# Optimization experiments

Measured on AMD Instinct MI355X. Metric: run time of the kernel, lower is better.

Reference implementation:

```python
import math
import jax, jax.numpy as jnp
import numpy as np


def setup_inputs() -> dict:
    key = jax.random.key(0)
    ks = jax.random.split(key, 5)
    B, T, C = 4, 2048, 1024
    H = 16
    s = 0.02
    return {
        "x": jax.random.normal(ks[0], (B, T, C), dtype=jnp.float32),
        "W_attn": jax.random.normal(ks[1], (C, 3 * C), dtype=jnp.float32) * s,
        "b_attn": jax.random.normal(ks[2], (3 * C,), dtype=jnp.float32) * s,
        "W_proj": jax.random.normal(ks[3], (C, C), dtype=jnp.float32) * s,
        "b_proj": jax.random.normal(ks[4], (C,), dtype=jnp.float32) * s,
        "n_head": 16,
    }


def reference(x, W_attn, b_attn, W_proj, b_proj, n_head):
    B, T, C = x.shape
    hd = C // n_head
    qkv = x @ W_attn + b_attn  # (B,T,3C)
    q, k, v = jnp.split(qkv, 3, axis=-1)
    # (B,H,T,hd)
    q = q.reshape(B, T, n_head, hd).transpose(0, 2, 1, 3)
    k = k.reshape(B, T, n_head, hd).transpose(0, 2, 1, 3)
    v = v.reshape(B, T, n_head, hd).transpose(0, 2, 1, 3)
    # ||q-k||^2 = |q|^2 + |k|^2 - 2 q.k  (GEMM form, avoids (B,H,T,T,hd) diff tensor)
    q2 = jnp.sum(q * q, axis=-1)[..., :, None]  # (B,H,T,1)
    k2 = jnp.sum(k * k, axis=-1)[..., None, :]  # (B,H,1,T)
    qk = jnp.einsum("bhqd,bhkd->bhqk", q, k)    # (B,H,T,T)
    sq_l2 = q2 + k2 - 2.0 * qk
    scale = -1.0 / (2.0 * math.sqrt(hd))
    scores = jnp.exp(sq_l2 * scale)
    causal = jnp.tril(jnp.ones((T, T), dtype=bool))  # (T,T)
    scores = jnp.where(causal[None, None, :, :], scores, 0.0)
    y = jnp.einsum("bhqk,bhkd->bhqd", scores, v)  # (B,H,T,hd)
    y = y.transpose(0, 2, 1, 3).reshape(B, T, C)
    return y @ W_proj + b_proj
```

## Files before the change

kernel.cpp:

```cpp
#include <hip/hip_runtime.h>

typedef __bf16 bf16;
typedef __bf16 bf16x8 __attribute__((ext_vector_type(8)));
typedef float floatx4 __attribute__((ext_vector_type(4)));

#define MFMA_BF16(a, b, c) __builtin_amdgcn_mfma_f32_16x16x32_bf16((a), (b), (c), 0, 0, 0)

#define GLOAD_LDS16(gp, lp)                                      \
  __builtin_amdgcn_global_load_lds(                              \
      (const __attribute__((address_space(1))) void*)(gp),       \
      (__attribute__((address_space(3))) void*)(lp), 16, 0, 0)

#define SEQ_T 2048
#define DIM_C 1024
#define HDIM 64
#define MROWS 8192
#define N_QKV 3072

__global__ __launch_bounds__(256) void f32_to_bf16(
    const float* __restrict__ in, bf16* __restrict__ out) {
  const size_t i = ((size_t)blockIdx.x * 256 + threadIdx.x) * 8;
  const float4 f0 = *(const float4*)&in[i];
  const float4 f1 = *(const float4*)&in[i + 4];
  bf16x8 v;
  v[0] = (bf16)f0.x; v[1] = (bf16)f0.y; v[2] = (bf16)f0.z; v[3] = (bf16)f0.w;
  v[4] = (bf16)f1.x; v[5] = (bf16)f1.y; v[6] = (bf16)f1.z; v[7] = (bf16)f1.w;
  *(bf16x8*)&out[i] = v;
}

__global__ __launch_bounds__(256) void transpose_f32_bf16(
    const float* __restrict__ in, bf16* __restrict__ out, int R, int C) {
  __shared__ bf16 tile[32][33];
  const int bx = blockIdx.x * 32, by = blockIdx.y * 32;
  const int tx = threadIdx.x & 31, ty = threadIdx.x >> 5;
  for (int i = 0; i < 32; i += 8)
    tile[ty + i][tx] = (bf16)in[(size_t)(by + ty + i) * C + bx + tx];
  __syncthreads();
  for (int i = 0; i < 32; i += 8)
    out[(size_t)(bx + ty + i) * R + by + tx] = tile[tx][ty + i];
}

template <typename OT>
__global__ __launch_bounds__(256) void gemm_lds(
    const bf16* __restrict__ A,
    const bf16* __restrict__ Bt,
    const float* __restrict__ bias,
    OT* __restrict__ Cout,
    int M, int N, int K) {
  __shared__ __align__(16) bf16 Asl[128 * 64];
  __shared__ __align__(16) bf16 Bsl[128 * 64];
  const int bm = blockIdx.y * 128, bn = blockIdx.x * 128;
  const int tid = threadIdx.x;
  const int wave = tid >> 6, lane = tid & 63;
  const int wm = (wave >> 1) * 64, wn = (wave & 1) * 64;
  const int quad = lane >> 4, l16 = lane & 15;

  const floatx4 zero = {0.f, 0.f, 0.f, 0.f};
  floatx4 acc[4][4];
  for (int i = 0; i < 4; i++)
    for (int j = 0; j < 4; j++) acc[i][j] = zero;

  const bf16 *gA[4], *gB[4];
  bf16 *lA[4], *lB[4];
  for (int i = 0; i < 4; i++) {
    const int s = i * 256 + tid;
    const int row = s >> 3;
    const int c = (s & 7) ^ (row & 7);
    gA[i] = &A[(size_t)(bm + row) * K + c * 8];
    gB[i] = &Bt[(size_t)(bn + row) * K + c * 8];
    lA[i] = &Asl[(i * 256 + wave * 64) * 8];
    lB[i] = &Bsl[(i * 256 + wave * 64) * 8];
  }

  for (int k0 = 0; k0 < K; k0 += 64) {
    for (int i = 0; i < 4; i++) GLOAD_LDS16(gA[i] + k0, lA[i]);
    for (int i = 0; i < 4; i++) GLOAD_LDS16(gB[i] + k0, lB[i]);
    __syncthreads();
    for (int kk = 0; kk < 2; kk++) {
      bf16x8 af[4], bfr[4];
      for (int it = 0; it < 4; it++) {
        const int row = wm + it * 16 + l16;
        const int phys = (kk * 4 + quad) ^ (row & 7);
        af[it] = *(const bf16x8*)&Asl[row * 64 + phys * 8];
      }
      for (int jt = 0; jt < 4; jt++) {
        const int row = wn + jt * 16 + l16;
        const int phys = (kk * 4 + quad) ^ (row & 7);
        bfr[jt] = *(const bf16x8*)&Bsl[row * 64 + phys * 8];
      }
      for (int it = 0; it < 4; it++)
        for (int jt = 0; jt < 4; jt++)
          acc[it][jt] = MFMA_BF16(af[it], bfr[jt], acc[it][jt]);
    }
    __syncthreads();
  }
  for (int jt = 0; jt < 4; jt++) {
    const int col = bn + wn + jt * 16 + l16;
    const float bv = bias[col];
    for (int it = 0; it < 4; it++)
      for (int r = 0; r < 4; r++) {
        const int row = bm + wm + it * 16 + quad * 4 + r;
        Cout[(size_t)row * N + col] = (OT)(acc[it][jt][r] + bv);
      }
  }
}

__global__ __launch_bounds__(256, 4) void attn_kernel(
    const bf16* __restrict__ qkv,
    bf16* __restrict__ y) {
  const int p = blockIdx.x;
  const int bh = blockIdx.y;
  const int bb = bh >> 4, h = bh & 15;
  const int qtA = p, qtB = 31 - p;
  const int tid = threadIdx.x;
  const int wave = tid >> 6, lane = tid & 63;
  const int quad = lane >> 4, l16 = lane & 15;

  __shared__ __align__(16) bf16 Ps[128][72];
  __shared__ __align__(16) bf16 Ks[64][72];
  __shared__ __align__(16) bf16 Vt[64][72];
  __shared__ float q2c[128];

  const size_t rowbase = (size_t)bb * SEQ_T;
  const float c2 = -0.09016844f;
  const float m2c2 = 0.18033688f;

  bf16x8 aq[2][2];
  for (int T = 0; T < 2; T++) {
    const int qt = T ? qtB : qtA;
    const size_t grow = rowbase + qt * 64 + wave * 16 + l16;
    float s = 0.f;
    for (int ks = 0; ks < 2; ks++) {
      aq[T][ks] = *(const bf16x8*)&qkv[grow * N_QKV + h * HDIM + ks * 32 + quad * 8];
      for (int j = 0; j < 8; j++) { const float f = (float)aq[T][ks][j]; s += f * f; }
    }
    s += __shfl_xor(s, 16); s += __shfl_xor(s, 32);
    if (quad == 0) q2c[T * 64 + wave * 16 + l16] = s * c2;
  }

  const floatx4 zero = {0.f, 0.f, 0.f, 0.f};
  floatx4 accy[2][4];
  for (int T = 0; T < 2; T++)
    for (int jt = 0; jt < 4; jt++) accy[T][jt] = zero;

  for (int kt = 0; kt <= qtB; kt++) {
    const bool actA = (kt <= qtA);
    {
      const int r0 = tid >> 3, c8 = (tid & 7) << 3;
      for (int i = 0; i < 2; i++) {
        const int r = r0 + i * 32;
        const size_t gr = rowbase + (size_t)(kt * 64 + r);
        const bf16x8 kv = *(const bf16x8*)&qkv[gr * N_QKV + 1024 + h * HDIM + c8];
        *(bf16x8*)&Ks[r][c8] = kv;
        float s = 0.f;
        for (int j = 0; j < 8; j++) { const float f = (float)kv[j]; s += f * f; }
        s += __shfl_xor(s, 1); s += __shfl_xor(s, 2); s += __shfl_xor(s, 4);
        const float vscale = exp2f(s * c2);
        const bf16x8 vv = *(const bf16x8*)&qkv[gr * N_QKV + 2048 + h * HDIM + c8];
        for (int j = 0; j < 8; j++)
          Vt[c8 + j][r ^ c8] = (bf16)((float)vv[j] * vscale);
      }
    }
    __syncthreads();

    bf16x8 bk[4][2];
    for (int jt = 0; jt < 4; jt++)
      for (int ks = 0; ks < 2; ks++)
        bk[jt][ks] = *(const bf16x8*)&Ks[jt * 16 + l16][ks * 32 + quad * 8];
    floatx4 accs[2][4];
    for (int T = 0; T < 2; T++)
      for (int jt = 0; jt < 4; jt++) accs[T][jt] = zero;
    for (int T = 0; T < 2; T++) {
      if (T == 0 && !actA) continue;
      for (int ks = 0; ks < 2; ks++)
        for (int jt = 0; jt < 4; jt++)
          accs[T][jt] = MFMA_BF16(aq[T][ks], bk[jt][ks], accs[T][jt]);
    }

    for (int T = 0; T < 2; T++) {
      if (T == 0 && !actA) continue;
      const bool diag = (kt == (T == 0 ? qtA : qtB));
      for (int jt = 0; jt < 4; jt++) {
        const int nl = jt * 16 + l16;
        for (int r = 0; r < 4; r++) {
          const int ml = wave * 16 + quad * 4 + r;
          float pe = exp2f(m2c2 * accs[T][jt][r]);
          if (diag && nl > ml) pe = 0.f;
          Ps[T * 64 + ml][nl] = (bf16)pe;
        }
      }
    }

    bf16x8 bv[4][2];
    for (int jt = 0; jt < 4; jt++)
      for (int ks = 0; ks < 2; ks++) {
        const int d = jt * 16 + l16;
        bv[jt][ks] = *(const bf16x8*)&Vt[d][(ks * 32 + quad * 8) ^ (d & 0x38)];
      }
    for (int T = 0; T < 2; T++) {
      if (T == 0 && !actA) continue;
      for (int ks = 0; ks < 2; ks++) {
        const bf16x8 ap =
            *(const bf16x8*)&Ps[T * 64 + wave * 16 + l16][ks * 32 + quad * 8];
        for (int jt = 0; jt < 4; jt++)
          accy[T][jt] = MFMA_BF16(ap, bv[jt][ks], accy[T][jt]);
      }
    }
    __syncthreads();
  }

  for (int T = 0; T < 2; T++) {
    const int qt = (T == 0) ? qtA : qtB;
    float ysc[4];
    for (int r = 0; r < 4; r++)
      ysc[r] = exp2f(q2c[T * 64 + wave * 16 + quad * 4 + r]);
    for (int jt = 0; jt < 4; jt++) {
      const int col = h * HDIM + jt * 16 + l16;
      for (int r = 0; r < 4; r++) {
        const int ml = wave * 16 + quad * 4 + r;
        y[(rowbase + qt * 64 + ml) * DIM_C + col] = (bf16)(accy[T][jt][r] * ysc[r]);
      }
    }
  }
}

extern "C" void kernel_launch(void* const* d_in, const int* in_sizes, int n_in,
                              void* d_out, int out_size, void* d_ws, size_t ws_size,
                              hipStream_t stream) {
  const float* x      = (const float*)d_in[0];
  const float* W_attn = (const float*)d_in[1];
  const float* b_attn = (const float*)d_in[2];
  const float* W_proj = (const float*)d_in[3];
  const float* b_proj = (const float*)d_in[4];
  float* out = (float*)d_out;

  char* ws = (char*)d_ws;
  bf16* qkv = (bf16*)(ws);
  bf16* yb  = (bf16*)(ws + 50331648);
  bf16* WaT = (bf16*)(ws + 67108864);
  bf16* WpT = (bf16*)(ws + 73400320);
  bf16* xb  = yb;

  f32_to_bf16<<<dim3(4096), 256, 0, stream>>>(x, xb);
  transpose_f32_bf16<<<dim3(96, 32), 256, 0, stream>>>(W_attn, WaT, 1024, 3072);
  transpose_f32_bf16<<<dim3(32, 32), 256, 0, stream>>>(W_proj, WpT, 1024, 1024);
  gemm_lds<bf16><<<dim3(24, 64), 256, 0, stream>>>(
      xb, WaT, b_attn, qkv, MROWS, N_QKV, DIM_C);
  attn_kernel<<<dim3(16, 64), 256, 0, stream>>>(qkv, yb);
  gemm_lds<float><<<dim3(8, 64), 256, 0, stream>>>(
      yb, WpT, b_proj, out, MROWS, DIM_C, DIM_C);
}
```

Baseline: 302.8 us.

## Keep attention probabilities in registers, feed PV via 16x16x16 MFMA

```diff
diff --git a/kernel.cpp b/kernel.cpp
--- a/kernel.cpp
+++ b/kernel.cpp
@@ -2,9 +2,20 @@
 
 typedef __bf16 bf16;
 typedef __bf16 bf16x8 __attribute__((ext_vector_type(8)));
+typedef __bf16 bf16x4 __attribute__((ext_vector_type(4)));
+typedef short shortx4 __attribute__((ext_vector_type(4)));
 typedef float floatx4 __attribute__((ext_vector_type(4)));
 
 #define MFMA_BF16(a, b, c) __builtin_amdgcn_mfma_f32_16x16x32_bf16((a), (b), (c), 0, 0, 0)
+
+#if __has_builtin(__builtin_amdgcn_mfma_f32_16x16x16_bf16)
+#define MFMA16(a, b, c) __builtin_amdgcn_mfma_f32_16x16x16_bf16((a), (b), (c), 0, 0, 0)
+#else
+#define MFMA16(a, b, c)                                                   \
+  __builtin_amdgcn_mfma_f32_16x16x16bf16_1k(                              \
+      __builtin_bit_cast(shortx4, (a)), __builtin_bit_cast(shortx4, (b)), \
+      (c), 0, 0, 0)
+#endif
 
 #define GLOAD_LDS16(gp, lp)                                      \
   __builtin_amdgcn_global_load_lds(                              \
@@ -116,7 +127,6 @@
   const int wave = tid >> 6, lane = tid & 63;
   const int quad = lane >> 4, l16 = lane & 15;
 
-  __shared__ __align__(16) bf16 Ps[128][72];
   __shared__ __align__(16) bf16 Ks[64][72];
   __shared__ __align__(16) bf16 Vt[64][72];
   __shared__ float q2c[128];
@@ -141,7 +151,7 @@
   const floatx4 zero = {0.f, 0.f, 0.f, 0.f};
   floatx4 accy[2][4];
   for (int T = 0; T < 2; T++)
-    for (int jt = 0; jt < 4; jt++) accy[T][jt] = zero;
+    for (int dt = 0; dt < 4; dt++) accy[T][dt] = zero;
 
   for (int kt = 0; kt <= qtB; kt++) {
     const bool actA = (kt <= qtA);
@@ -164,47 +174,60 @@
     __syncthreads();
 
     bf16x8 bk[4][2];
+#pragma unroll
     for (int jt = 0; jt < 4; jt++)
+#pragma unroll
       for (int ks = 0; ks < 2; ks++)
         bk[jt][ks] = *(const bf16x8*)&Ks[jt * 16 + l16][ks * 32 + quad * 8];
     floatx4 accs[2][4];
+#pragma unroll
     for (int T = 0; T < 2; T++)
+#pragma unroll
       for (int jt = 0; jt < 4; jt++) accs[T][jt] = zero;
+#pragma unroll
     for (int T = 0; T < 2; T++) {
       if (T == 0 && !actA) continue;
+#pragma unroll
       for (int ks = 0; ks < 2; ks++)
+#pragma unroll
         for (int jt = 0; jt < 4; jt++)
-          accs[T][jt] = MFMA_BF16(aq[T][ks], bk[jt][ks], accs[T][jt]);
-    }
-
+          accs[T][jt] = MFMA_BF16(bk[jt][ks], aq[T][ks], accs[T][jt]);
+    }
+
+    bf16x4 ap[2][4];
+    const int qrow = wave * 16 + l16;
+#pragma unroll
     for (int T = 0; T < 2; T++) {
       if (T == 0 && !actA) continue;
       const bool diag = (kt == (T == 0 ? qtA : qtB));
+#pragma unroll
       for (int jt = 0; jt < 4; jt++) {
-        const int nl = jt * 16 + l16;
+        const int kb = jt * 16 + quad * 4;
+#pragma unroll
         for (int r = 0; r < 4; r++) {
-          const int ml = wave * 16 + quad * 4 + r;
           float pe = exp2f(m2c2 * accs[T][jt][r]);
-          if (diag && nl > ml) pe = 0.f;
-          Ps[T * 64 + ml][nl] = (bf16)pe;
+          if (diag && kb + r > qrow) pe = 0.f;
+          ap[T][jt][r] = (bf16)pe;
         }
       }
     }
 
-    bf16x8 bv[4][2];
-    for (int jt = 0; jt < 4; jt++)
-      for (int ks = 0; ks < 2; ks++) {
-        const int d = jt * 16 + l16;
-        bv[jt][ks] = *(const bf16x8*)&Vt[d][(ks * 32 + quad * 8) ^ (d & 0x38)];
-      }
-    for (int T = 0; T < 2; T++) {
-      if (T == 0 && !actA) continue;
-      for (int ks = 0; ks < 2; ks++) {
-        const bf16x8 ap =
-            *(const bf16x8*)&Ps[T * 64 + wave * 16 + l16][ks * 32 + quad * 8];
-        for (int jt = 0; jt < 4; jt++)
-          accy[T][jt] = MFMA_BF16(ap, bv[jt][ks], accy[T][jt]);
-      }
+#pragma unroll
+    for (int dt = 0; dt < 4; dt++) {
+      const int d = dt * 16 + l16;
+      const int swz = d & 0x38;
+      bf16x4 bv[4];
+#pragma unroll
+      for (int ksl = 0; ksl < 4; ksl++)
+        bv[ksl] = *(const bf16x4*)&Vt[d][(ksl * 16 + quad * 4) ^ swz];
+      if (actA) {
+#pragma unroll
+        for (int ksl = 0; ksl < 4; ksl++)
+          accy[0][dt] = MFMA16(ap[0][ksl], bv[ksl], accy[0][dt]);
+      }
+#pragma unroll
+      for (int ksl = 0; ksl < 4; ksl++)
+        accy[1][dt] = MFMA16(ap[1][ksl], bv[ksl], accy[1][dt]);
     }
     __syncthreads();
   }
@@ -214,11 +237,11 @@
     float ysc[4];
     for (int r = 0; r < 4; r++)
       ysc[r] = exp2f(q2c[T * 64 + wave * 16 + quad * 4 + r]);
-    for (int jt = 0; jt < 4; jt++) {
-      const int col = h * HDIM + jt * 16 + l16;
+    for (int dt = 0; dt < 4; dt++) {
+      const int col = h * HDIM + dt * 16 + l16;
       for (int r = 0; r < 4; r++) {
         const int ml = wave * 16 + quad * 4 + r;
-        y[(rowbase + qt * 64 + ml) * DIM_C + col] = (bf16)(accy[T][jt][r] * ysc[r]);
+        y[(rowbase + qt * 64 + ml) * DIM_C + col] = (bf16)(accy[T][dt][r] * ysc[r]);
       }
     }
   }
```

Result: slower. 353.2 us (+16.7%).

## Precompute scaled transposed V and double-buffer K/V loads in attention

Applied to the files above, without the earlier changes.

```diff
diff --git a/kernel.cpp b/kernel.cpp
--- a/kernel.cpp
+++ b/kernel.cpp
@@ -2,6 +2,7 @@
 
 typedef __bf16 bf16;
 typedef __bf16 bf16x8 __attribute__((ext_vector_type(8)));
+typedef __bf16 bf16x4 __attribute__((ext_vector_type(4)));
 typedef float floatx4 __attribute__((ext_vector_type(4)));
 
 #define MFMA_BF16(a, b, c) __builtin_amdgcn_mfma_f32_16x16x32_bf16((a), (b), (c), 0, 0, 0)
@@ -40,13 +41,43 @@
     out[(size_t)(bx + ty + i) * R + by + tx] = tile[tx][ty + i];
 }
 
+__global__ __launch_bounds__(256) void scale_transpose_v(
+    const bf16* __restrict__ qkv, bf16* __restrict__ VT) {
+  const int bh = blockIdx.x;
+  const int kt = blockIdx.y;
+  const int bb = bh >> 4, h = bh & 15;
+  const int tid = threadIdx.x;
+  __shared__ bf16 tile[64][72];
+  const int r0 = tid >> 3, c8 = (tid & 7) << 3;
+  const float c2 = -0.09016844f;
+  for (int i = 0; i < 2; i++) {
+    const int r = r0 + i * 32;
+    const size_t gr = (size_t)bb * SEQ_T + kt * 64 + r;
+    const bf16x8 kv = *(const bf16x8*)&qkv[gr * N_QKV + 1024 + h * HDIM + c8];
+    float s = 0.f;
+    for (int j = 0; j < 8; j++) { const float f = (float)kv[j]; s += f * f; }
+    s += __shfl_xor(s, 1); s += __shfl_xor(s, 2); s += __shfl_xor(s, 4);
+    const float vscale = exp2f(s * c2);
+    const bf16x8 vv = *(const bf16x8*)&qkv[gr * N_QKV + 2048 + h * HDIM + c8];
+    for (int j = 0; j < 8; j++)
+      tile[c8 + j][r ^ c8] = (bf16)((float)vv[j] * vscale);
+  }
+  __syncthreads();
+  for (int i = 0; i < 2; i++) {
+    const int u = i * 256 + tid;
+    const int d = u >> 3, kc = (u & 7) << 3;
+    const bf16x8 ov = *(const bf16x8*)&tile[d][kc ^ (d & 0x38)];
+    *(bf16x8*)&VT[(size_t)bh * 131072 + (size_t)d * 2048 + kt * 64 + kc] = ov;
+  }
+}
+
 template <typename OT>
 __global__ __launch_bounds__(256) void gemm_lds(
     const bf16* __restrict__ A,
     const bf16* __restrict__ Bt,
     const float* __restrict__ bias,
     OT* __restrict__ Cout,
-    int M, int N, int K) {
+    int M, int N, int K, int lda) {
   __shared__ __align__(16) bf16 Asl[128 * 64];
   __shared__ __align__(16) bf16 Bsl[128 * 64];
   const int bm = blockIdx.y * 128, bn = blockIdx.x * 128;
@@ -66,7 +97,7 @@
     const int s = i * 256 + tid;
     const int row = s >> 3;
     const int c = (s & 7) ^ (row & 7);
-    gA[i] = &A[(size_t)(bm + row) * K + c * 8];
+    gA[i] = &A[(size_t)(bm + row) * lda + c * 8];
     gB[i] = &Bt[(size_t)(bn + row) * K + c * 8];
     lA[i] = &Asl[(i * 256 + wave * 64) * 8];
     lB[i] = &Bsl[(i * 256 + wave * 64) * 8];
@@ -106,10 +137,10 @@
 }
 
 __global__ __launch_bounds__(256, 4) void attn_kernel(
-    const bf16* __restrict__ qkv,
-    bf16* __restrict__ y) {
-  const int p = blockIdx.x;
-  const int bh = blockIdx.y;
+    bf16* __restrict__ qkv,
+    const bf16* __restrict__ VT) {
+  const int p = blockIdx.y;
+  const int bh = blockIdx.x;
   const int bb = bh >> 4, h = bh & 15;
   const int qtA = p, qtB = 31 - p;
   const int tid = threadIdx.x;
@@ -117,8 +148,8 @@
   const int quad = lane >> 4, l16 = lane & 15;
 
   __shared__ __align__(16) bf16 Ps[128][72];
-  __shared__ __align__(16) bf16 Ks[64][72];
-  __shared__ __align__(16) bf16 Vt[64][72];
+  __shared__ __align__(16) bf16 Ksl[2][64 * 64];
+  __shared__ __align__(16) bf16 Vsl[2][64 * 64];
   __shared__ float q2c[128];
 
   const size_t rowbase = (size_t)bb * SEQ_T;
@@ -143,30 +174,38 @@
   for (int T = 0; T < 2; T++)
     for (int jt = 0; jt < 4; jt++) accy[T][jt] = zero;
 
+  const int r0 = tid >> 3;
+  const int cb = (tid & 7) ^ (r0 & 7);
+  const bf16* gK = &qkv[(rowbase + r0) * N_QKV + 1024 + h * HDIM + cb * 8];
+  const bf16* gV = &VT[(size_t)bh * 131072 + (size_t)r0 * 2048 + cb * 8];
+
+#define STAGE(kt_, nb_) do {                                            \
+    const size_t ko = (size_t)(kt_) * 64 * N_QKV;                       \
+    const int vo = (kt_) * 64;                                          \
+    GLOAD_LDS16(gK + ko,                    &Ksl[nb_][(wave * 64) * 8]);\
+    GLOAD_LDS16(gK + ko + (size_t)32 * N_QKV,                           \
+                &Ksl[nb_][(256 + wave * 64) * 8]);                      \
+    GLOAD_LDS16(gV + vo,                    &Vsl[nb_][(wave * 64) * 8]);\
+    GLOAD_LDS16(gV + vo + 32 * 2048,        &Vsl[nb_][(256 + wave * 64) * 8]);\
+  } while (0)
+
+  STAGE(0, 0);
+  int cur = 0;
+  const int qrow = wave * 16 + l16;
+
   for (int kt = 0; kt <= qtB; kt++) {
     const bool actA = (kt <= qtA);
-    {
-      const int r0 = tid >> 3, c8 = (tid & 7) << 3;
-      for (int i = 0; i < 2; i++) {
-        const int r = r0 + i * 32;
-        const size_t gr = rowbase + (size_t)(kt * 64 + r);
-        const bf16x8 kv = *(const bf16x8*)&qkv[gr * N_QKV + 1024 + h * HDIM + c8];
-        *(bf16x8*)&Ks[r][c8] = kv;
-        float s = 0.f;
-        for (int j = 0; j < 8; j++) { const float f = (float)kv[j]; s += f * f; }
-        s += __shfl_xor(s, 1); s += __shfl_xor(s, 2); s += __shfl_xor(s, 4);
-        const float vscale = exp2f(s * c2);
-        const bf16x8 vv = *(const bf16x8*)&qkv[gr * N_QKV + 2048 + h * HDIM + c8];
-        for (int j = 0; j < 8; j++)
-          Vt[c8 + j][r ^ c8] = (bf16)((float)vv[j] * vscale);
-      }
-    }
     __syncthreads();
+    if (kt < qtB) STAGE(kt + 1, cur ^ 1);
+    const bf16* Kb = Ksl[cur];
+    const bf16* Vb = Vsl[cur];
 
     bf16x8 bk[4][2];
     for (int jt = 0; jt < 4; jt++)
-      for (int ks = 0; ks < 2; ks++)
-        bk[jt][ks] = *(const bf16x8*)&Ks[jt * 16 + l16][ks * 32 + quad * 8];
+      for (int ks = 0; ks < 2; ks++) {
+        const int phys = (ks * 4 + quad) ^ (l16 & 7);
+        bk[jt][ks] = *(const bf16x8*)&Kb[(jt * 16 + l16) * 64 + phys * 8];
+      }
     floatx4 accs[2][4];
     for (int T = 0; T < 2; T++)
       for (int jt = 0; jt < 4; jt++) accs[T][jt] = zero;
@@ -174,40 +213,42 @@
       if (T == 0 && !actA) continue;
       for (int ks = 0; ks < 2; ks++)
         for (int jt = 0; jt < 4; jt++)
-          accs[T][jt] = MFMA_BF16(aq[T][ks], bk[jt][ks], accs[T][jt]);
+          accs[T][jt] = MFMA_BF16(bk[jt][ks], aq[T][ks], accs[T][jt]);
     }
 
     for (int T = 0; T < 2; T++) {
       if (T == 0 && !actA) continue;
       const bool diag = (kt == (T == 0 ? qtA : qtB));
       for (int jt = 0; jt < 4; jt++) {
-        const int nl = jt * 16 + l16;
+        const int kb = jt * 16 + quad * 4;
+        bf16x4 pw;
         for (int r = 0; r < 4; r++) {
-          const int ml = wave * 16 + quad * 4 + r;
           float pe = exp2f(m2c2 * accs[T][jt][r]);
-          if (diag && nl > ml) pe = 0.f;
-          Ps[T * 64 + ml][nl] = (bf16)pe;
+          if (diag && kb + r > qrow) pe = 0.f;
+          pw[r] = (bf16)pe;
         }
+        *(bf16x4*)&Ps[T * 64 + qrow][kb] = pw;
       }
     }
 
     bf16x8 bv[4][2];
-    for (int jt = 0; jt < 4; jt++)
+    for (int dt = 0; dt < 4; dt++)
       for (int ks = 0; ks < 2; ks++) {
-        const int d = jt * 16 + l16;
-        bv[jt][ks] = *(const bf16x8*)&Vt[d][(ks * 32 + quad * 8) ^ (d & 0x38)];
+        const int phys = (ks * 4 + quad) ^ (l16 & 7);
+        bv[dt][ks] = *(const bf16x8*)&Vb[(dt * 16 + l16) * 64 + phys * 8];
       }
     for (int T = 0; T < 2; T++) {
       if (T == 0 && !actA) continue;
       for (int ks = 0; ks < 2; ks++) {
         const bf16x8 ap =
-            *(const bf16x8*)&Ps[T * 64 + wave * 16 + l16][ks * 32 + quad * 8];
+            *(const bf16x8*)&Ps[T * 64 + qrow][ks * 32 + quad * 8];
         for (int jt = 0; jt < 4; jt++)
           accy[T][jt] = MFMA_BF16(ap, bv[jt][ks], accy[T][jt]);
       }
     }
-    __syncthreads();
-  }
+    cur ^= 1;
+  }
+#undef STAGE
 
   for (int T = 0; T < 2; T++) {
     const int qt = (T == 0) ? qtA : qtB;
@@ -218,7 +259,8 @@
       const int col = h * HDIM + jt * 16 + l16;
       for (int r = 0; r < 4; r++) {
         const int ml = wave * 16 + quad * 4 + r;
-        y[(rowbase + qt * 64 + ml) * DIM_C + col] = (bf16)(accy[T][jt][r] * ysc[r]);
+        qkv[(rowbase + qt * 64 + ml) * N_QKV + 2048 + col] =
+            (bf16)(accy[T][jt][r] * ysc[r]);
       }
     }
   }
@@ -236,17 +278,18 @@
 
   char* ws = (char*)d_ws;
   bf16* qkv = (bf16*)(ws);
-  bf16* yb  = (bf16*)(ws + 50331648);
+  bf16* VTb = (bf16*)(ws + 50331648);
   bf16* WaT = (bf16*)(ws + 67108864);
   bf16* WpT = (bf16*)(ws + 73400320);
-  bf16* xb  = yb;
+  bf16* xb  = VTb;
 
   f32_to_bf16<<<dim3(4096), 256, 0, stream>>>(x, xb);
   transpose_f32_bf16<<<dim3(96, 32), 256, 0, stream>>>(W_attn, WaT, 1024, 3072);
   transpose_f32_bf16<<<dim3(32, 32), 256, 0, stream>>>(W_proj, WpT, 1024, 1024);
   gemm_lds<bf16><<<dim3(24, 64), 256, 0, stream>>>(
-      xb, WaT, b_attn, qkv, MROWS, N_QKV, DIM_C);
-  attn_kernel<<<dim3(16, 64), 256, 0, stream>>>(qkv, yb);
+      xb, WaT, b_attn, qkv, MROWS, N_QKV, DIM_C, DIM_C);
+  scale_transpose_v<<<dim3(64, 32), 256, 0, stream>>>(qkv, VTb);
+  attn_kernel<<<dim3(64, 16), 256, 0, stream>>>(qkv, VTb);
   gemm_lds<float><<<dim3(8, 64), 256, 0, stream>>>(
-      yb, WpT, b_proj, out, MROWS, DIM_C, DIM_C);
-}
+      qkv + 2048, WpT, b_proj, out, MROWS, DIM_C, DIM_C, N_QKV);
+}
```

Result: faster. 289.5 us (-4.4%).
